# Kernel optimization log

Measured on AMD Instinct MI355X. Metric: run time of the kernel, lower is better.

Reference implementation:

```python
import jax, jax.numpy as jnp
import numpy as np
from jax import lax

WBITS = 2
ABITS = 2
STRIDES = (1, 1)
PADDING = 'SAME'


def _ste_quantize(x, k):
    # round(x * n) / n with straight-through gradient (identity)
    n = float(2 ** k - 1)
    q = jnp.round(x * n) / n
    return x + lax.stop_gradient(q - x)


def _quantize_weight(w, k):
    # DoReFa-style weight quantization: tanh, normalize to [0,1], quantize, map to [-1,1]
    t = jnp.tanh(w)
    t = t / jnp.max(jnp.abs(t)) * 0.5 + 0.5
    return 2.0 * _ste_quantize(t, k) - 1.0


def _quantize_act(x, k):
    return _ste_quantize(jnp.clip(x, 0.0, 1.0), k)


def setup_inputs() -> dict:
    key = jax.random.key(0)
    kx, kw = jax.random.split(key)
    x = jax.random.uniform(kx, (32, 56, 56, 256), dtype=jnp.float32)  # NHWC
    w = jax.random.normal(kw, (3, 3, 256, 256), dtype=jnp.float32) * 0.2  # HWIO
    # match init normalization: unit L2 norm per output channel over (h,w,cin)
    w = w / jnp.sqrt(1e-7 + jnp.sum(w * w, axis=(0, 1, 2), keepdims=True))
    return {'x': x, 'w': w}


def reference(x, w) -> jnp.ndarray:
    wq = _quantize_weight(w, WBITS)        # low-bit weights in [-1, 1]
    xq = _quantize_act(x, ABITS)           # low-bit activations in [0, 1]
    out = lax.conv_general_dilated(
        xq, wq,
        window_strides=STRIDES,
        padding=PADDING,
        dimension_numbers=('NHWC', 'HWIO', 'NHWC'),
    )
    return out
```

## Files before the change

### kernel.cpp

```cpp
#include <hip/hip_runtime.h>
#include <stdint.h>

#define GLOBAL_AS __attribute__((address_space(1)))
#define LDS_AS    __attribute__((address_space(3)))

typedef int v4i __attribute__((ext_vector_type(4)));

__device__ __forceinline__ void gload_lds16(const void* g, void* l) {
    __builtin_amdgcn_global_load_lds((GLOBAL_AS uint32_t*)g, (LDS_AS uint32_t*)l, 16, 0, 0);
}

__global__ void k_wmax(const float* __restrict__ w, unsigned* __restrict__ maxbits, int n) {
    int i = blockIdx.x * blockDim.x + threadIdx.x;
    int stride = gridDim.x * blockDim.x;
    float m = 0.f;
    for (; i < n; i += stride) m = fmaxf(m, fabsf(tanhf(w[i])));
#pragma unroll
    for (int off = 32; off > 0; off >>= 1)
        m = fmaxf(m, __shfl_xor(m, off, 64));
    if ((threadIdx.x & 63) == 0) atomicMax(maxbits, __float_as_uint(m));
}

__global__ void k_wq(const float* __restrict__ w, const unsigned* __restrict__ maxbits,
                     int8_t* __restrict__ wqt) {
    int t = blockIdx.x * 256 + threadIdx.x;
    int co = t / 2304;
    int k  = t - co * 2304;
    float ma = __uint_as_float(*maxbits);
    float tv = tanhf(w[(long)k * 256 + co]);
    float tq = tv / ma * 0.5f + 0.5f;
    int qi = (int)rintf(tq * 3.0f);
    wqt[t] = (int8_t)(2 * qi - 3);
}

__global__ void k_xq(const float* __restrict__ x, int8_t* __restrict__ xqp) {
    int t = blockIdx.x * 256 + threadIdx.x;
    int g  = t & 15;
    int p  = t >> 4;
    int xp = p % 58;
    int q  = p / 58;
    int yp = q % 58;
    int n  = q / 58;
    int4 r;
    if (yp == 0 || yp == 57 || xp == 0 || xp == 57) {
        r = make_int4(0, 0, 0, 0);
    } else {
        const float4* px = (const float4*)(x + (((long)((n * 56 + (yp - 1)) * 56 + (xp - 1))) << 8) + g * 16);
        int wds[4];
#pragma unroll
        for (int jj = 0; jj < 4; ++jj) {
            float4 v = px[jj];
            int b0 = (int)rintf(fminf(fmaxf(v.x, 0.f), 1.f) * 3.f);
            int b1 = (int)rintf(fminf(fmaxf(v.y, 0.f), 1.f) * 3.f);
            int b2 = (int)rintf(fminf(fmaxf(v.z, 0.f), 1.f) * 3.f);
            int b3 = (int)rintf(fminf(fmaxf(v.w, 0.f), 1.f) * 3.f);
            wds[jj] = b0 | (b1 << 8) | (b2 << 16) | (b3 << 24);
        }
        r = make_int4(wds[0], wds[1], wds[2], wds[3]);
    }
    *(int4*)(xqp + ((long)t << 4)) = r;
}

#define BM 128
#define BN 128

__global__ __launch_bounds__(256) void k_conv(const int8_t* __restrict__ xqp,
                                              const int8_t* __restrict__ wqt,
                                              float* __restrict__ out) {
    __shared__ int8_t sA[BM * 64];
    __shared__ int8_t sB[BN * 64];

    const int tid    = threadIdx.x;
    const int wv     = tid >> 6;
    const int lane   = tid & 63;
    const int mBase  = blockIdx.x * BM;
    const int coBase = blockIdx.y * BN;

    const int lq = lane >> 2;
    const int lb = (lane & 3) * 16;
    const int8_t* aPtr[2];
    const int8_t* bPtr[2];
#pragma unroll
    for (int j = 0; j < 2; ++j) {
        int i = wv * 32 + j * 16 + lq;
        int m = mBase + i;
        int n = m / 3136;
        int r = m - n * 3136;
        int y = r / 56;
        int x = r - y * 56;
        aPtr[j] = xqp + (((long)((n * 58 + y) * 58 + x)) << 8) + lb;
        int cl = coBase + wv * 32 + j * 16 + lq;
        bPtr[j] = wqt + (long)cl * 2304 + lb;
    }
    int8_t* sAw = sA + (wv * 32) * 64;
    int8_t* sBw = sB + (wv * 32) * 64;

    v4i acc[4][4];
#pragma unroll
    for (int a = 0; a < 4; ++a)
#pragma unroll
        for (int b = 0; b < 4; ++b) acc[a][b] = (v4i){0, 0, 0, 0};

    const int wm   = (wv & 1) * 64;
    const int wn   = (wv >> 1) * 64;
    const int frow = lane & 15;
    const int fq16 = (lane >> 4) * 16;

    for (int tap = 0; tap < 9; ++tap) {
        const int ky = tap / 3;
        const int kx = tap - ky * 3;
        const int aoffTap = ((ky * 58) + kx) << 8;
        const int boffTap = tap << 8;
#pragma unroll
        for (int cc = 0; cc < 4; ++cc) {
            __syncthreads();
            const int ao = aoffTap + cc * 64;
            const int bo = boffTap + cc * 64;
            gload_lds16(aPtr[0] + ao, sAw);
            gload_lds16(aPtr[1] + ao, sAw + 1024);
            gload_lds16(bPtr[0] + bo, sBw);
            gload_lds16(bPtr[1] + bo, sBw + 1024);
            __syncthreads();

            v4i af[4], bf[4];
#pragma unroll
            for (int mt = 0; mt < 4; ++mt)
                af[mt] = *(const v4i*)(sA + (wm + mt * 16 + frow) * 64 + fq16);
#pragma unroll
            for (int nt = 0; nt < 4; ++nt)
                bf[nt] = *(const v4i*)(sB + (wn + nt * 16 + frow) * 64 + fq16);
#pragma unroll
            for (int mt = 0; mt < 4; ++mt)
#pragma unroll
                for (int nt = 0; nt < 4; ++nt)
                    acc[mt][nt] = __builtin_amdgcn_mfma_i32_16x16x64_i8(af[mt], bf[nt], acc[mt][nt], 0, 0, 0);
        }
    }

    const float s = 1.0f / 9.0f;
    const int colB  = coBase + wn + frow;
    const int rquad = (lane >> 4) * 4;
#pragma unroll
    for (int mt = 0; mt < 4; ++mt) {
#pragma unroll
        for (int nt = 0; nt < 4; ++nt) {
            const int col = colB + nt * 16;
            const long mrow = mBase + wm + mt * 16 + rquad;
#pragma unroll
            for (int r = 0; r < 4; ++r)
                out[(mrow + r) * 256 + col] = (float)acc[mt][nt][r] * s;
        }
    }
}

extern "C" void kernel_launch(void* const* d_in, const int* in_sizes, int n_in,
                              void* d_out, int out_size, void* d_ws, size_t ws_size,
                              hipStream_t stream) {
    const float* x = (const float*)d_in[0];
    const float* w = (const float*)d_in[1];
    float* out = (float*)d_out;

    unsigned* maxbits = (unsigned*)d_ws;
    int8_t* wqt = (int8_t*)d_ws + 4096;
    int8_t* xqp = (int8_t*)d_ws + 4096 + 589824;

    hipMemsetAsync(maxbits, 0, 4, stream);
    k_wmax<<<256, 256, 0, stream>>>(w, maxbits, 3 * 3 * 256 * 256);
    k_wq<<<2304, 256, 0, stream>>>(w, maxbits, wqt);
    k_xq<<<6728, 256, 0, stream>>>(x, xqp);
    dim3 grid(784, 2);
    k_conv<<<grid, 256, 0, stream>>>(xqp, wqt, out);
}
```

Before: 282.9 us.

## Use 32x32x32 int8 MFMA with 128-byte K chunks and XOR-swizzled LDS

```diff
diff --git a/kernel.cpp b/kernel.cpp
--- a/kernel.cpp
+++ b/kernel.cpp
@@ -4,7 +4,8 @@
 #define GLOBAL_AS __attribute__((address_space(1)))
 #define LDS_AS    __attribute__((address_space(3)))
 
-typedef int v4i __attribute__((ext_vector_type(4)));
+typedef int v4i  __attribute__((ext_vector_type(4)));
+typedef int v16i __attribute__((ext_vector_type(16)));
 
 __device__ __forceinline__ void gload_lds16(const void* g, void* l) {
     __builtin_amdgcn_global_load_lds((GLOBAL_AS uint32_t*)g, (LDS_AS uint32_t*)l, 16, 0, 0);
@@ -24,13 +25,17 @@
 __global__ void k_wq(const float* __restrict__ w, const unsigned* __restrict__ maxbits,
                      int8_t* __restrict__ wqt) {
     int t = blockIdx.x * 256 + threadIdx.x;
-    int co = t / 2304;
-    int k  = t - co * 2304;
-    float ma = __uint_as_float(*maxbits);
-    float tv = tanhf(w[(long)k * 256 + co]);
-    float tq = tv / ma * 0.5f + 0.5f;
-    int qi = (int)rintf(tq * 3.0f);
-    wqt[t] = (int8_t)(2 * qi - 3);
+    int co = t & 255;
+    int kblk = t >> 8;
+    float inv = 0.5f / __uint_as_float(*maxbits);
+    int8_t b[16];
+#pragma unroll
+    for (int i = 0; i < 16; ++i) {
+        float tv = tanhf(w[(long)(kblk * 16 + i) * 256 + co]);
+        int qi = (int)rintf((tv * inv + 0.5f) * 3.0f);
+        b[i] = (int8_t)(2 * qi - 3);
+    }
+    *(int4*)(wqt + (long)co * 2304 + kblk * 16) = *(int4*)b;
 }
 
 __global__ void k_xq(const float* __restrict__ x, int8_t* __restrict__ xqp) {
@@ -67,8 +72,8 @@
 __global__ __launch_bounds__(256) void k_conv(const int8_t* __restrict__ xqp,
                                               const int8_t* __restrict__ wqt,
                                               float* __restrict__ out) {
-    __shared__ int8_t sA[BM * 64];
-    __shared__ int8_t sB[BN * 64];
+    __shared__ int8_t sA[BM * 128];
+    __shared__ int8_t sB[BN * 128];
 
     const int tid    = threadIdx.x;
     const int wv     = tid >> 6;
@@ -76,79 +81,85 @@
     const int mBase  = blockIdx.x * BM;
     const int coBase = blockIdx.y * BN;
 
-    const int lq = lane >> 2;
-    const int lb = (lane & 3) * 16;
-    const int8_t* aPtr[2];
-    const int8_t* bPtr[2];
+    const int lr = lane >> 3;
+    const int lp = lane & 7;
+    const int8_t* aB[4];
+    const int8_t* bB[4];
 #pragma unroll
-    for (int j = 0; j < 2; ++j) {
-        int i = wv * 32 + j * 16 + lq;
-        int m = mBase + i;
+    for (int j = 0; j < 4; ++j) {
+        int r = wv * 8 + j * 32 + lr;
+        int g = lp ^ (r & 7);
+        int m = mBase + r;
         int n = m / 3136;
-        int r = m - n * 3136;
-        int y = r / 56;
-        int x = r - y * 56;
-        aPtr[j] = xqp + (((long)((n * 58 + y) * 58 + x)) << 8) + lb;
-        int cl = coBase + wv * 32 + j * 16 + lq;
-        bPtr[j] = wqt + (long)cl * 2304 + lb;
+        int rem = m - n * 3136;
+        int y = rem / 56;
+        int x = rem - y * 56;
+        aB[j] = xqp + (((long)((n * 58 + y) * 58 + x)) << 8) + g * 16;
+        bB[j] = wqt + (long)(coBase + r) * 2304 + g * 16;
     }
-    int8_t* sAw = sA + (wv * 32) * 64;
-    int8_t* sBw = sB + (wv * 32) * 64;
 
-    v4i acc[4][4];
+    v16i acc[2][2];
 #pragma unroll
-    for (int a = 0; a < 4; ++a)
+    for (int a = 0; a < 2; ++a)
 #pragma unroll
-        for (int b = 0; b < 4; ++b) acc[a][b] = (v4i){0, 0, 0, 0};
+        for (int b = 0; b < 2; ++b)
+#pragma unroll
+            for (int r = 0; r < 16; ++r) acc[a][b][r] = 0;
 
-    const int wm   = (wv & 1) * 64;
-    const int wn   = (wv >> 1) * 64;
-    const int frow = lane & 15;
-    const int fq16 = (lane >> 4) * 16;
+    const int wm  = (wv & 1) * 64;
+    const int wn  = (wv >> 1) * 64;
+    const int l31 = lane & 31;
+    const int hi  = lane >> 5;
 
-    for (int tap = 0; tap < 9; ++tap) {
-        const int ky = tap / 3;
-        const int kx = tap - ky * 3;
-        const int aoffTap = ((ky * 58) + kx) << 8;
-        const int boffTap = tap << 8;
+    const int rA0 = wm + l31,      rA1 = wm + 32 + l31;
+    const int rB0 = wn + l31,      rB1 = wn + 32 + l31;
+    const int8_t* aF0 = sA + rA0 * 128;  const int axr0 = (rA0 & 7) << 4;
+    const int8_t* aF1 = sA + rA1 * 128;  const int axr1 = (rA1 & 7) << 4;
+    const int8_t* bF0 = sB + rB0 * 128;  const int bxr0 = (rB0 & 7) << 4;
+    const int8_t* bF1 = sB + rB1 * 128;  const int bxr1 = (rB1 & 7) << 4;
+
+    for (int iter = 0; iter < 18; ++iter) {
+        const int tap  = iter >> 1;
+        const int ky   = tap / 3;
+        const int kx   = tap - ky * 3;
+        const int half = (iter & 1) * 128;
+        const int aOff = (((ky * 58) + kx) << 8) + half;
+        const int bOff = tap * 256 + half;
+
+        __syncthreads();
 #pragma unroll
-        for (int cc = 0; cc < 4; ++cc) {
-            __syncthreads();
-            const int ao = aoffTap + cc * 64;
-            const int bo = boffTap + cc * 64;
-            gload_lds16(aPtr[0] + ao, sAw);
-            gload_lds16(aPtr[1] + ao, sAw + 1024);
-            gload_lds16(bPtr[0] + bo, sBw);
-            gload_lds16(bPtr[1] + bo, sBw + 1024);
-            __syncthreads();
+        for (int j = 0; j < 4; ++j) {
+            gload_lds16(aB[j] + aOff, sA + (wv * 8 + j * 32) * 128);
+            gload_lds16(bB[j] + bOff, sB + (wv * 8 + j * 32) * 128);
+        }
+        __syncthreads();
 
-            v4i af[4], bf[4];
 #pragma unroll
-            for (int mt = 0; mt < 4; ++mt)
-                af[mt] = *(const v4i*)(sA + (wm + mt * 16 + frow) * 64 + fq16);
-#pragma unroll
-            for (int nt = 0; nt < 4; ++nt)
-                bf[nt] = *(const v4i*)(sB + (wn + nt * 16 + frow) * 64 + fq16);
-#pragma unroll
-            for (int mt = 0; mt < 4; ++mt)
-#pragma unroll
-                for (int nt = 0; nt < 4; ++nt)
-                    acc[mt][nt] = __builtin_amdgcn_mfma_i32_16x16x64_i8(af[mt], bf[nt], acc[mt][nt], 0, 0, 0);
+        for (int kk = 0; kk < 4; ++kk) {
+            const int kc = (kk * 2 + hi) << 4;
+            v4i a0 = *(const v4i*)(aF0 + (kc ^ axr0));
+            v4i a1 = *(const v4i*)(aF1 + (kc ^ axr1));
+            v4i b0 = *(const v4i*)(bF0 + (kc ^ bxr0));
+            v4i b1 = *(const v4i*)(bF1 + (kc ^ bxr1));
+            acc[0][0] = __builtin_amdgcn_mfma_i32_32x32x32_i8(a0, b0, acc[0][0], 0, 0, 0);
+            acc[0][1] = __builtin_amdgcn_mfma_i32_32x32x32_i8(a0, b1, acc[0][1], 0, 0, 0);
+            acc[1][0] = __builtin_amdgcn_mfma_i32_32x32x32_i8(a1, b0, acc[1][0], 0, 0, 0);
+            acc[1][1] = __builtin_amdgcn_mfma_i32_32x32x32_i8(a1, b1, acc[1][1], 0, 0, 0);
         }
     }
 
     const float s = 1.0f / 9.0f;
-    const int colB  = coBase + wn + frow;
-    const int rquad = (lane >> 4) * 4;
 #pragma unroll
-    for (int mt = 0; mt < 4; ++mt) {
+    for (int mt = 0; mt < 2; ++mt) {
 #pragma unroll
-        for (int nt = 0; nt < 4; ++nt) {
-            const int col = colB + nt * 16;
-            const long mrow = mBase + wm + mt * 16 + rquad;
+        for (int nt = 0; nt < 2; ++nt) {
+            const int ocol = coBase + wn + nt * 32 + l31;
 #pragma unroll
-            for (int r = 0; r < 4; ++r)
-                out[(mrow + r) * 256 + col] = (float)acc[mt][nt][r] * s;
+            for (int reg = 0; reg < 16; ++reg) {
+                const int row = (reg & 3) + 8 * (reg >> 2) + 4 * hi;
+                const long orow = mBase + wm + mt * 32 + row;
+                out[orow * 256 + ocol] = (float)acc[mt][nt][reg] * s;
+            }
         }
     }
 }
@@ -166,7 +177,7 @@
 
     hipMemsetAsync(maxbits, 0, 4, stream);
     k_wmax<<<256, 256, 0, stream>>>(w, maxbits, 3 * 3 * 256 * 256);
-    k_wq<<<2304, 256, 0, stream>>>(w, maxbits, wqt);
+    k_wq<<<144, 256, 0, stream>>>(w, maxbits, wqt);
     k_xq<<<6728, 256, 0, stream>>>(x, xqp);
     dim3 grid(784, 2);
     k_conv<<<grid, 256, 0, stream>>>(xqp, wqt, out);
```

New measurement: 275.7 us. 1.03x faster.
